# Optimization experiments

Measured on AMD Instinct MI355X. Metric: run time of the kernel, lower is better.

The kernel has to match this reference:

```python
import math
import jax, jax.numpy as jnp
import numpy as np

N_NODES = 50000
N_EDGES = 800000
IN_F = 128
OUT_F = 64


def setup_inputs() -> dict:
    key = jax.random.key(0)
    k1, k2, k3, k4 = jax.random.split(key, 4)
    x = jax.random.normal(k1, (N_NODES, IN_F), dtype=jnp.float32)
    edge_index = jax.random.randint(k2, (2, N_EDGES), 0, N_NODES, dtype=jnp.int64)
    # Linear weights, torch layout [out_features, in_features], Kaiming-uniform-like scale
    bound = 1.0 / math.sqrt(IN_F)
    Wq = jax.random.uniform(k3, (OUT_F, IN_F), dtype=jnp.float32, minval=-bound, maxval=bound)
    Wk = jax.random.uniform(k4, (OUT_F, IN_F), dtype=jnp.float32, minval=-bound, maxval=bound)
    return {"x": x, "edge_index": edge_index, "Wq": Wq, "Wk": Wk}


def reference(x, edge_index, Wq, Wk):
    scale = math.sqrt(OUT_F)
    Q = x @ Wq.T  # [N, F]
    K = x @ Wk.T  # [N, F]
    row, col = edge_index[0], edge_index[1]
    # per-edge scaled dot-product attention logits
    alpha = jnp.sum(Q[row] * K[col], axis=-1) / scale  # [E]
    # segment softmax grouped by destination node (col)
    seg_max = jax.ops.segment_max(alpha, col, num_segments=N_NODES)  # [N]
    # empty segments give -inf max; those segments have no edges so exp is never used there
    ex = jnp.exp(alpha - seg_max[col])  # [E]
    denom = jax.ops.segment_sum(ex, col, num_segments=N_NODES)  # [N]
    alpha = ex / (denom[col] + 1e-16)  # [E]
    # dropout p=0 (eval) -> identity
    # weighted scatter-add of source Q features into destination nodes
    out = jax.ops.segment_sum(Q[row] * alpha[:, None], col, num_segments=N_NODES)  # [N, F]
    return out
```

## Files before the change

### kernel.cpp

```cpp
#include <hip/hip_runtime.h>
#include <math.h>

#define N_NODES 50000
#define N_EDGES 800000
#define IN_F 128
#define OUT_F 64

#define NBUK 196
#define BCAP 5120
#define BIN_CHUNK 2048
#define BIN_BLOCKS ((N_EDGES + BIN_CHUNK - 1) / BIN_CHUNK)
#define QK_NB 64
#define QK_BLOCKS ((N_NODES + QK_NB - 1) / QK_NB)

typedef __attribute__((ext_vector_type(8))) short short8v;
typedef __attribute__((ext_vector_type(4))) float f32x4;

__device__ __forceinline__ unsigned short bf16_rne(float f) {
    unsigned u = __float_as_uint(f);
    return (unsigned short)((u + 0x7FFFu + ((u >> 16) & 1u)) >> 16);
}
__device__ __forceinline__ void split2(float f, unsigned short& h, unsigned short& l) {
    h = bf16_rne(f);
    float fh = __uint_as_float(((unsigned)h) << 16);
    l = bf16_rne(f - fh);
}
__device__ __forceinline__ float bf2f(ushort h) {
    return __uint_as_float(((unsigned)h) << 16);
}

__global__ __launch_bounds__(256) void wsplit(const float* __restrict__ Wq,
                                              const float* __restrict__ Wk,
                                              const int* __restrict__ ei,
                                              ushort* __restrict__ wh,
                                              ushort* __restrict__ wl,
                                              int* __restrict__ bcnt,
                                              int* __restrict__ offs,
                                              int* __restrict__ eflag) {
    int i = blockIdx.x * 256 + threadIdx.x;
    if (blockIdx.x == 0 && threadIdx.x < NBUK) bcnt[threadIdx.x] = 0;
    if (blockIdx.x == 0 && threadIdx.x == 0) {
        offs[N_NODES] = N_EDGES;
        int allz = 1;
        for (int k = 0; k < 32; ++k)
            if (ei[2 * k + 1] != 0) allz = 0;
        *eflag = allz;
    }
    if (i >= 2 * OUT_F * IN_F) return;
    float f = (i < OUT_F * IN_F) ? Wq[i] : Wk[i - OUT_F * IN_F];
    unsigned short h, l;
    split2(f, h, l);
    wh[i] = h;
    wl[i] = l;
}

__global__ __launch_bounds__(256) void bin_edges(const void* __restrict__ ei,
                                                 const int* __restrict__ eflag,
                                                 int* __restrict__ bcnt,
                                                 unsigned* __restrict__ binned) {
    __shared__ unsigned recbuf[BIN_CHUNK];
    __shared__ int cnt[NBUK];
    __shared__ int gbase[NBUK];
    const int t = threadIdx.x;
    const int sflag = *eflag;
    for (int i = t; i < NBUK; i += 256) cnt[i] = 0;
    __syncthreads();

    const int e0 = blockIdx.x * BIN_CHUNK;
    const int nloc = min(BIN_CHUNK, N_EDGES - e0);
    for (int i = t; i < nloc; i += 256) {
        int e = e0 + i;
        int r, c;
        if (sflag) {
            const long long* p = (const long long*)ei;
            r = (int)p[e];
            c = (int)p[N_EDGES + e];
        } else {
            const int* p = (const int*)ei;
            r = p[e];
            c = p[N_EDGES + e];
        }
        unsigned rec = (unsigned)r | ((unsigned)c << 16);
        recbuf[i] = rec;
        atomicAdd(&cnt[c >> 8], 1);
    }
    __syncthreads();
    for (int i = t; i < NBUK; i += 256) {
        gbase[i] = atomicAdd(&bcnt[i], cnt[i]);
        cnt[i] = 0;
    }
    __syncthreads();
    for (int i = t; i < nloc; i += 256) {
        unsigned rec = recbuf[i];
        int b = rec >> 24;
        int lp = atomicAdd(&cnt[b], 1);
        int pos = gbase[b] + lp;
        if (pos >= BCAP) pos = BCAP - 1;
        binned[(size_t)b * BCAP + pos] = rec;
    }
}

__global__ __launch_bounds__(256, 2) void fat_qk_bucket(const float* __restrict__ x,
                                                        const ushort* __restrict__ wh,
                                                        const ushort* __restrict__ wl,
                                                        ushort* __restrict__ Qh,
                                                        ushort* __restrict__ Kh,
                                                        const unsigned* __restrict__ binned,
                                                        const int* __restrict__ bcnt,
                                                        int* __restrict__ offs,
                                                        ushort* __restrict__ sorted_row) {
    __shared__ __align__(16) char smem[65536];
    const int t = threadIdx.x;

    if (blockIdx.x < NBUK) {
        int* colcnt = (int*)smem;
        int* colhead = (int*)(smem + 1024);
        int* s = (int*)(smem + 2048);
        ushort* image = (ushort*)(smem + 3072);
        const int b = blockIdx.x;
        const int c0 = b << 8;
        const int cntb = bcnt[b];
        const unsigned* slab = binned + (size_t)b * BCAP;

        s[t] = (t < b) ? bcnt[t] : 0;
        __syncthreads();
        for (int off = 128; off > 0; off >>= 1) {
            if (t < off) s[t] += s[t + off];
            __syncthreads();
        }
        const int baseb = s[0];
        __syncthreads();

        colcnt[t] = 0;
        __syncthreads();
        for (int i = t; i < cntb; i += 256)
            atomicAdd(&colcnt[(slab[i] >> 16) & 0xFF], 1);
        __syncthreads();
        s[t] = colcnt[t];
        __syncthreads();
        for (int off = 1; off < 256; off <<= 1) {
            int u = (t >= off) ? s[t - off] : 0;
            __syncthreads();
            s[t] += u;
            __syncthreads();
        }
        const int excl = s[t] - colcnt[t];
        colhead[t] = excl;
        if (c0 + t < N_NODES) offs[c0 + t] = baseb + excl;
        __syncthreads();
        for (int i = t; i < cntb; i += 256) {
            unsigned rec = slab[i];
            int p = atomicAdd(&colhead[(rec >> 16) & 0xFF], 1);
            image[p] = (ushort)(rec & 0xFFFF);
        }
        __syncthreads();
        for (int i = t; i < cntb; i += 256)
            sorted_row[baseb + i] = image[i];
        return;
    }

    char* lds0 = smem;
    for (int u = t; u < 4096; u += 256) {
        int mh = u >> 10;
        int j = (u >> 4) & 63;
        int kb = u & 15;
        const ushort* src = (mh & 1) ? wl : wh;
        int soff = ((mh >> 1) << 13) + (j << 7) + (kb << 3);
        short8v v = *(const short8v*)(src + soff);
        unsigned byte = ((unsigned)u * 16u) ^ (((unsigned)j & 7u) << 4);
        *(short8v*)(lds0 + byte) = v;
    }

    const int w = t >> 6, l = t & 63;
    const int base = (blockIdx.x - NBUK) * QK_NB + w * 16;
    const int lr = l & 15, kg = l >> 4;

    int nodeA = base + lr;
    if (nodeA >= N_NODES) nodeA = N_NODES - 1;
    const float* xp = x + (size_t)nodeA * IN_F + kg * 8;

    short8v ah[4], al[4];
#pragma unroll
    for (int ks = 0; ks < 4; ++ks) {
        float4 a0 = *(const float4*)(xp + ks * 32);
        float4 a1 = *(const float4*)(xp + ks * 32 + 4);
        float v[8] = {a0.x, a0.y, a0.z, a0.w, a1.x, a1.y, a1.z, a1.w};
#pragma unroll
        for (int jj = 0; jj < 8; ++jj) {
            unsigned short h, lo;
            split2(v[jj], h, lo);
            ah[ks][jj] = (short)h;
            al[ks][jj] = (short)lo;
        }
    }

    __syncthreads();

#pragma unroll
    for (int mat = 0; mat < 2; ++mat) {
        ushort* O = mat ? Kh : Qh;
#pragma unroll
        for (int nt = 0; nt < 4; ++nt) {
            const int j = nt * 16 + lr;
            const unsigned swz = (((unsigned)j & 7u) << 4);
            const unsigned bh_base = (unsigned)((mat * 2 + 0) * 64 + j) * 256u;
            const unsigned bl_base = (unsigned)((mat * 2 + 1) * 64 + j) * 256u;
            f32x4 acc = {0.0f, 0.0f, 0.0f, 0.0f};
#pragma unroll
            for (int ks = 0; ks < 4; ++ks) {
                unsigned off = ((unsigned)kg << 4) + ((unsigned)ks << 6);
                short8v bh = *(const short8v*)(lds0 + ((bh_base + off) ^ swz));
                short8v bl = *(const short8v*)(lds0 + ((bl_base + off) ^ swz));
                acc = __builtin_amdgcn_mfma_f32_16x16x32_bf16(ah[ks], bh, acc, 0, 0, 0);
                acc = __builtin_amdgcn_mfma_f32_16x16x32_bf16(ah[ks], bl, acc, 0, 0, 0);
                acc = __builtin_amdgcn_mfma_f32_16x16x32_bf16(al[ks], bh, acc, 0, 0, 0);
            }
            const int rowb = base + kg * 4;
#pragma unroll
            for (int r = 0; r < 4; ++r) {
                int node = rowb + r;
                if (node < N_NODES) O[(size_t)node * OUT_F + j] = bf16_rne(acc[r]);
            }
        }
    }
}

__global__ __launch_bounds__(256) void gat_node(const ushort* __restrict__ Qh,
                                                const ushort* __restrict__ Kh,
                                                const ushort* __restrict__ sorted_row,
                                                const int* __restrict__ offs,
                                                float* __restrict__ out) {
    const int wave = threadIdx.x >> 6, lane = threadIdx.x & 63;
    const int n = blockIdx.x * 4 + wave;
    if (n >= N_NODES) return;
    const int g = lane >> 4, gl = lane & 15;
    const int start = offs[n], deg = offs[n + 1] - start;

    const float C = 1.44269504f * 0.125f;
    const ushort4 kh = *(const ushort4*)(Kh + (size_t)n * OUT_F + gl * 4);
    const float kx = bf2f(kh.x) * C, ky = bf2f(kh.y) * C;
    const float kz = bf2f(kh.z) * C, kw = bf2f(kh.w) * C;

    float d0 = 0.0f, d1 = 0.0f;
    float4 o0 = {0.0f, 0.0f, 0.0f, 0.0f};
    float4 o1 = {0.0f, 0.0f, 0.0f, 0.0f};

    int i = g;
    for (; i + 4 < deg; i += 8) {
        int r0 = (int)sorted_row[start + i];
        int r1 = (int)sorted_row[start + i + 4];
        ushort4 qh0 = *(const ushort4*)(Qh + (size_t)r0 * OUT_F + gl * 4);
        ushort4 qh1 = *(const ushort4*)(Qh + (size_t)r1 * OUT_F + gl * 4);
        float q0x = bf2f(qh0.x), q0y = bf2f(qh0.y), q0z = bf2f(qh0.z), q0w = bf2f(qh0.w);
        float q1x = bf2f(qh1.x), q1y = bf2f(qh1.y), q1z = bf2f(qh1.z), q1w = bf2f(qh1.w);
        float p0 = q0x * kx + q0y * ky + q0z * kz + q0w * kw;
        float p1 = q1x * kx + q1y * ky + q1z * kz + q1w * kw;
        p0 += __shfl_xor(p0, 1);
        p1 += __shfl_xor(p1, 1);
        p0 += __shfl_xor(p0, 2);
        p1 += __shfl_xor(p1, 2);
        p0 += __shfl_xor(p0, 4);
        p1 += __shfl_xor(p1, 4);
        p0 += __shfl_xor(p0, 8);
        p1 += __shfl_xor(p1, 8);
        float e0 = exp2f(p0);
        float e1 = exp2f(p1);
        d0 += e0;
        d1 += e1;
        o0.x += e0 * q0x;
        o0.y += e0 * q0y;
        o0.z += e0 * q0z;
        o0.w += e0 * q0w;
        o1.x += e1 * q1x;
        o1.y += e1 * q1y;
        o1.z += e1 * q1z;
        o1.w += e1 * q1w;
    }
    if (i < deg) {
        int r0 = (int)sorted_row[start + i];
        ushort4 qh0 = *(const ushort4*)(Qh + (size_t)r0 * OUT_F + gl * 4);
        float q0x = bf2f(qh0.x), q0y = bf2f(qh0.y), q0z = bf2f(qh0.z), q0w = bf2f(qh0.w);
        float p0 = q0x * kx + q0y * ky + q0z * kz + q0w * kw;
        p0 += __shfl_xor(p0, 1);
        p0 += __shfl_xor(p0, 2);
        p0 += __shfl_xor(p0, 4);
        p0 += __shfl_xor(p0, 8);
        float e0 = exp2f(p0);
        d0 += e0;
        o0.x += e0 * q0x;
        o0.y += e0 * q0y;
        o0.z += e0 * q0z;
        o0.w += e0 * q0w;
    }

    d0 += d1;
    o0.x += o1.x;
    o0.y += o1.y;
    o0.z += o1.z;
    o0.w += o1.w;

#pragma unroll
    for (int off = 16; off <= 32; off <<= 1) {
        d0 += __shfl_xor(d0, off);
        o0.x += __shfl_xor(o0.x, off);
        o0.y += __shfl_xor(o0.y, off);
        o0.z += __shfl_xor(o0.z, off);
        o0.w += __shfl_xor(o0.w, off);
    }

    if (g == 0) {
        float inv = 1.0f / (d0 + 1e-16f);
        float4 r = {o0.x * inv, o0.y * inv, o0.z * inv, o0.w * inv};
        *(float4*)(out + (size_t)n * OUT_F + gl * 4) = r;
    }
}

extern "C" void kernel_launch(void* const* d_in, const int* in_sizes, int n_in,
                              void* d_out, int out_size, void* d_ws, size_t ws_size,
                              hipStream_t stream) {
    const float* x = (const float*)d_in[0];
    const void* ei = d_in[1];
    const float* Wq = (const float*)d_in[2];
    const float* Wk = (const float*)d_in[3];
    float* out = (float*)d_out;

    char* ws = (char*)d_ws;
    ushort* Qh = (ushort*)ws;         ws += (size_t)N_NODES * OUT_F * 2;
    ushort* Kh = (ushort*)ws;         ws += (size_t)N_NODES * OUT_F * 2;
    unsigned* binned = (unsigned*)ws; ws += (size_t)NBUK * BCAP * 4;
    ushort* sorted_row = (ushort*)ws; ws += (size_t)N_EDGES * 2;
    ushort* wh = (ushort*)ws;         ws += (size_t)2 * OUT_F * IN_F * 2;
    ushort* wl = (ushort*)ws;         ws += (size_t)2 * OUT_F * IN_F * 2;
    ws = (char*)(((size_t)ws + 255) & ~(size_t)255);
    int* bcnt = (int*)ws;             ws += (size_t)NBUK * 4;
    int* offs = (int*)ws;             ws += (size_t)(N_NODES + 1) * 4;
    int* eflag = (int*)ws;            ws += 256;

    wsplit<<<(2 * OUT_F * IN_F + 255) / 256, 256, 0, stream>>>(Wq, Wk, (const int*)ei,
                                                               wh, wl, bcnt, offs, eflag);
    bin_edges<<<BIN_BLOCKS, 256, 0, stream>>>(ei, eflag, bcnt, binned);
    fat_qk_bucket<<<NBUK + QK_BLOCKS, 256, 0, stream>>>(x, wh, wl, Qh, Kh,
                                                        binned, bcnt, offs, sorted_row);
    gat_node<<<(N_NODES + 3) / 4, 256, 0, stream>>>(Qh, Kh, sorted_row, offs, out);
}
```

Measured before the change: 74.46 us.

## Split Q/K GEMM across bin and bucket kernels to overlap with edge sorting

The fused Q+K projection is split into two halves. The Q half now runs in the same launch as edge binning, and the K half runs alongside the bucket sort, so GEMM work overlaps with the latency-bound sorting phases. This rebalances work across the launches and halves LDS per block (32KB), which may raise occupancy. In exchange, x is read and converted to bf16 hi/lo twice, once per kernel.

Measured after the change: 73.38 us. No clear change (-1.4%).

```diff
diff --git a/kernel.cpp b/kernel.cpp
--- a/kernel.cpp
+++ b/kernel.cpp
@@ -54,62 +54,137 @@
     wl[i] = l;
 }
 
-__global__ __launch_bounds__(256) void bin_edges(const void* __restrict__ ei,
-                                                 const int* __restrict__ eflag,
-                                                 int* __restrict__ bcnt,
-                                                 unsigned* __restrict__ binned) {
-    __shared__ unsigned recbuf[BIN_CHUNK];
-    __shared__ int cnt[NBUK];
-    __shared__ int gbase[NBUK];
+__device__ __forceinline__ void qk_gemm_half(const float* __restrict__ x,
+                                             const ushort* __restrict__ whm,
+                                             const ushort* __restrict__ wlm,
+                                             ushort* __restrict__ Oh,
+                                             char* lds0, int qbid, int t) {
+    for (int u = t; u < 2048; u += 256) {
+        int hl = u >> 10;
+        int j = (u >> 4) & 63;
+        int kb = u & 15;
+        const ushort* src = hl ? wlm : whm;
+        short8v v = *(const short8v*)(src + (j << 7) + (kb << 3));
+        unsigned byte = ((unsigned)u * 16u) ^ (((unsigned)j & 7u) << 4);
+        *(short8v*)(lds0 + byte) = v;
+    }
+
+    const int w = t >> 6, l = t & 63;
+    const int base = qbid * QK_NB + w * 16;
+    const int lr = l & 15, kg = l >> 4;
+
+    int nodeA = base + lr;
+    if (nodeA >= N_NODES) nodeA = N_NODES - 1;
+    const float* xp = x + (size_t)nodeA * IN_F + kg * 8;
+
+    short8v ah[4], al[4];
+#pragma unroll
+    for (int ks = 0; ks < 4; ++ks) {
+        float4 a0 = *(const float4*)(xp + ks * 32);
+        float4 a1 = *(const float4*)(xp + ks * 32 + 4);
+        float v[8] = {a0.x, a0.y, a0.z, a0.w, a1.x, a1.y, a1.z, a1.w};
+#pragma unroll
+        for (int jj = 0; jj < 8; ++jj) {
+            unsigned short h, lo;
+            split2(v[jj], h, lo);
+            ah[ks][jj] = (short)h;
+            al[ks][jj] = (short)lo;
+        }
+    }
+
+    __syncthreads();
+
+#pragma unroll
+    for (int nt = 0; nt < 4; ++nt) {
+        const int j = nt * 16 + lr;
+        const unsigned swz = (((unsigned)j & 7u) << 4);
+        const unsigned bh_base = (unsigned)j * 256u;
+        const unsigned bl_base = 16384u + (unsigned)j * 256u;
+        f32x4 acc = {0.0f, 0.0f, 0.0f, 0.0f};
+#pragma unroll
+        for (int ks = 0; ks < 4; ++ks) {
+            unsigned off = ((unsigned)kg << 4) + ((unsigned)ks << 6);
+            short8v bh = *(const short8v*)(lds0 + ((bh_base + off) ^ swz));
+            short8v bl = *(const short8v*)(lds0 + ((bl_base + off) ^ swz));
+            acc = __builtin_amdgcn_mfma_f32_16x16x32_bf16(ah[ks], bh, acc, 0, 0, 0);
+            acc = __builtin_amdgcn_mfma_f32_16x16x32_bf16(ah[ks], bl, acc, 0, 0, 0);
+            acc = __builtin_amdgcn_mfma_f32_16x16x32_bf16(al[ks], bh, acc, 0, 0, 0);
+        }
+        const int rowb = base + kg * 4;
+#pragma unroll
+        for (int r = 0; r < 4; ++r) {
+            int node = rowb + r;
+            if (node < N_NODES) Oh[(size_t)node * OUT_F + j] = bf16_rne(acc[r]);
+        }
+    }
+}
+
+__global__ __launch_bounds__(256, 2) void fat_bin_qkq(const void* __restrict__ ei,
+                                                      const int* __restrict__ eflag,
+                                                      int* __restrict__ bcnt,
+                                                      unsigned* __restrict__ binned,
+                                                      const float* __restrict__ x,
+                                                      const ushort* __restrict__ wh,
+                                                      const ushort* __restrict__ wl,
+                                                      ushort* __restrict__ Qh) {
+    __shared__ __align__(16) char smem[32768];
     const int t = threadIdx.x;
-    const int sflag = *eflag;
-    for (int i = t; i < NBUK; i += 256) cnt[i] = 0;
-    __syncthreads();
-
-    const int e0 = blockIdx.x * BIN_CHUNK;
-    const int nloc = min(BIN_CHUNK, N_EDGES - e0);
-    for (int i = t; i < nloc; i += 256) {
-        int e = e0 + i;
-        int r, c;
-        if (sflag) {
-            const long long* p = (const long long*)ei;
-            r = (int)p[e];
-            c = (int)p[N_EDGES + e];
-        } else {
-            const int* p = (const int*)ei;
-            r = p[e];
-            c = p[N_EDGES + e];
-        }
-        unsigned rec = (unsigned)r | ((unsigned)c << 16);
-        recbuf[i] = rec;
-        atomicAdd(&cnt[c >> 8], 1);
-    }
-    __syncthreads();
-    for (int i = t; i < NBUK; i += 256) {
-        gbase[i] = atomicAdd(&bcnt[i], cnt[i]);
-        cnt[i] = 0;
-    }
-    __syncthreads();
-    for (int i = t; i < nloc; i += 256) {
-        unsigned rec = recbuf[i];
-        int b = rec >> 24;
-        int lp = atomicAdd(&cnt[b], 1);
-        int pos = gbase[b] + lp;
-        if (pos >= BCAP) pos = BCAP - 1;
-        binned[(size_t)b * BCAP + pos] = rec;
-    }
-}
-
-__global__ __launch_bounds__(256, 2) void fat_qk_bucket(const float* __restrict__ x,
-                                                        const ushort* __restrict__ wh,
-                                                        const ushort* __restrict__ wl,
-                                                        ushort* __restrict__ Qh,
-                                                        ushort* __restrict__ Kh,
-                                                        const unsigned* __restrict__ binned,
-                                                        const int* __restrict__ bcnt,
-                                                        int* __restrict__ offs,
-                                                        ushort* __restrict__ sorted_row) {
-    __shared__ __align__(16) char smem[65536];
+
+    if (blockIdx.x < BIN_BLOCKS) {
+        unsigned* recbuf = (unsigned*)smem;
+        int* cnt = (int*)(smem + BIN_CHUNK * 4);
+        int* gbase = (int*)(smem + BIN_CHUNK * 4 + 1024);
+        const int sflag = *eflag;
+        for (int i = t; i < NBUK; i += 256) cnt[i] = 0;
+        __syncthreads();
+
+        const int e0 = blockIdx.x * BIN_CHUNK;
+        const int nloc = min(BIN_CHUNK, N_EDGES - e0);
+        for (int i = t; i < nloc; i += 256) {
+            int e = e0 + i;
+            int r, c;
+            if (sflag) {
+                const long long* p = (const long long*)ei;
+                r = (int)p[e];
+                c = (int)p[N_EDGES + e];
+            } else {
+                const int* p = (const int*)ei;
+                r = p[e];
+                c = p[N_EDGES + e];
+            }
+            unsigned rec = (unsigned)r | ((unsigned)c << 16);
+            recbuf[i] = rec;
+            atomicAdd(&cnt[c >> 8], 1);
+        }
+        __syncthreads();
+        for (int i = t; i < NBUK; i += 256) {
+            gbase[i] = atomicAdd(&bcnt[i], cnt[i]);
+            cnt[i] = 0;
+        }
+        __syncthreads();
+        for (int i = t; i < nloc; i += 256) {
+            unsigned rec = recbuf[i];
+            int b = rec >> 24;
+            int lp = atomicAdd(&cnt[b], 1);
+            int pos = gbase[b] + lp;
+            if (pos >= BCAP) pos = BCAP - 1;
+            binned[(size_t)b * BCAP + pos] = rec;
+        }
+        return;
+    }
+
+    qk_gemm_half(x, wh, wl, Qh, smem, blockIdx.x - BIN_BLOCKS, t);
+}
+
+__global__ __launch_bounds__(256, 2) void fat_bucket_qkk(const unsigned* __restrict__ binned,
+                                                         const int* __restrict__ bcnt,
+                                                         int* __restrict__ offs,
+                                                         ushort* __restrict__ sorted_row,
+                                                         const float* __restrict__ x,
+                                                         const ushort* __restrict__ wh,
+                                                         const ushort* __restrict__ wl,
+                                                         ushort* __restrict__ Kh) {
+    __shared__ __align__(16) char smem[32768];
     const int t = threadIdx.x;
 
     if (blockIdx.x < NBUK) {
@@ -159,70 +234,8 @@
         return;
     }
 
-    char* lds0 = smem;
-    for (int u = t; u < 4096; u += 256) {
-        int mh = u >> 10;
-        int j = (u >> 4) & 63;
-        int kb = u & 15;
-        const ushort* src = (mh & 1) ? wl : wh;
-        int soff = ((mh >> 1) << 13) + (j << 7) + (kb << 3);
-        short8v v = *(const short8v*)(src + soff);
-        unsigned byte = ((unsigned)u * 16u) ^ (((unsigned)j & 7u) << 4);
-        *(short8v*)(lds0 + byte) = v;
-    }
-
-    const int w = t >> 6, l = t & 63;
-    const int base = (blockIdx.x - NBUK) * QK_NB + w * 16;
-    const int lr = l & 15, kg = l >> 4;
-
-    int nodeA = base + lr;
-    if (nodeA >= N_NODES) nodeA = N_NODES - 1;
-    const float* xp = x + (size_t)nodeA * IN_F + kg * 8;
-
-    short8v ah[4], al[4];
-#pragma unroll
-    for (int ks = 0; ks < 4; ++ks) {
-        float4 a0 = *(const float4*)(xp + ks * 32);
-        float4 a1 = *(const float4*)(xp + ks * 32 + 4);
-        float v[8] = {a0.x, a0.y, a0.z, a0.w, a1.x, a1.y, a1.z, a1.w};
-#pragma unroll
-        for (int jj = 0; jj < 8; ++jj) {
-            unsigned short h, lo;
-            split2(v[jj], h, lo);
-            ah[ks][jj] = (short)h;
-            al[ks][jj] = (short)lo;
-        }
-    }
-
-    __syncthreads();
-
-#pragma unroll
-    for (int mat = 0; mat < 2; ++mat) {
-        ushort* O = mat ? Kh : Qh;
-#pragma unroll
-        for (int nt = 0; nt < 4; ++nt) {
-            const int j = nt * 16 + lr;
-            const unsigned swz = (((unsigned)j & 7u) << 4);
-            const unsigned bh_base = (unsigned)((mat * 2 + 0) * 64 + j) * 256u;
-            const unsigned bl_base = (unsigned)((mat * 2 + 1) * 64 + j) * 256u;
-            f32x4 acc = {0.0f, 0.0f, 0.0f, 0.0f};
-#pragma unroll
-            for (int ks = 0; ks < 4; ++ks) {
-                unsigned off = ((unsigned)kg << 4) + ((unsigned)ks << 6);
-                short8v bh = *(const short8v*)(lds0 + ((bh_base + off) ^ swz));
-                short8v bl = *(const short8v*)(lds0 + ((bl_base + off) ^ swz));
-                acc = __builtin_amdgcn_mfma_f32_16x16x32_bf16(ah[ks], bh, acc, 0, 0, 0);
-                acc = __builtin_amdgcn_mfma_f32_16x16x32_bf16(ah[ks], bl, acc, 0, 0, 0);
-                acc = __builtin_amdgcn_mfma_f32_16x16x32_bf16(al[ks], bh, acc, 0, 0, 0);
-            }
-            const int rowb = base + kg * 4;
-#pragma unroll
-            for (int r = 0; r < 4; ++r) {
-                int node = rowb + r;
-                if (node < N_NODES) O[(size_t)node * OUT_F + j] = bf16_rne(acc[r]);
-            }
-        }
-    }
+    qk_gemm_half(x, wh + OUT_F * IN_F, wl + OUT_F * IN_F, Kh, smem,
+                 blockIdx.x - NBUK, t);
 }
 
 __global__ __launch_bounds__(256) void gat_node(const ushort* __restrict__ Qh,
@@ -338,8 +351,9 @@
 
     wsplit<<<(2 * OUT_F * IN_F + 255) / 256, 256, 0, stream>>>(Wq, Wk, (const int*)ei,
                                                                wh, wl, bcnt, offs, eflag);
-    bin_edges<<<BIN_BLOCKS, 256, 0, stream>>>(ei, eflag, bcnt, binned);
-    fat_qk_bucket<<<NBUK + QK_BLOCKS, 256, 0, stream>>>(x, wh, wl, Qh, Kh,
-                                                        binned, bcnt, offs, sorted_row);
+    fat_bin_qkq<<<BIN_BLOCKS + QK_BLOCKS, 256, 0, stream>>>(ei, eflag, bcnt, binned,
+                                                            x, wh, wl, Qh);
+    fat_bucket_qkk<<<NBUK + QK_BLOCKS, 256, 0, stream>>>(binned, bcnt, offs, sorted_row,
+                                                         x, wh, wl, Kh);
     gat_node<<<(N_NODES + 3) / 4, 256, 0, stream>>>(Qh, Kh, sorted_row, offs, out);
 }
```
